# Kernel optimization log

Hardware: AMD Instinct MI355X
Metric: run time of the kernel (lower is better)

## Reference

```python
import jax, jax.numpy as jnp
import numpy as np

B, N, K = 4, 1024, 32
C_S, C_Z, C_H, H, PQ, PV = 384, 128, 16, 12, 4, 8
INF, EPS = 1e5, 1e-8
LN_EPS = 1e-5


def _quat_to_rot(q):
    # q: [..., 4] unit quaternions -> [..., 3, 3]
    w, x, y, z = q[..., 0], q[..., 1], q[..., 2], q[..., 3]
    r = jnp.stack([
        1 - 2 * (y * y + z * z), 2 * (x * y - w * z), 2 * (x * z + w * y),
        2 * (x * y + w * z), 1 - 2 * (x * x + z * z), 2 * (y * z - w * x),
        2 * (x * z - w * y), 2 * (y * z + w * x), 1 - 2 * (x * x + y * y),
    ], axis=-1)
    return r.reshape(q.shape[:-1] + (3, 3))


def _layernorm(x, scale, bias):
    m = jnp.mean(x, axis=-1, keepdims=True)
    v = jnp.mean((x - m) ** 2, axis=-1, keepdims=True)
    return (x - m) * jax.lax.rsqrt(v + LN_EPS) * scale + bias


def setup_inputs():
    key = jax.random.key(0)
    ks = jax.random.split(key, 16)
    s = jax.random.normal(ks[0], (B, N, C_S), jnp.float32)
    z = jax.random.normal(ks[1], (B, N, K, C_Z), jnp.float32)
    edge_index = jax.random.randint(ks[2], (B, N, K), 0, N, jnp.int32)
    quat = jax.random.normal(ks[3], (B, N, 4), jnp.float32)
    rot = _quat_to_rot(quat / jnp.linalg.norm(quat, axis=-1, keepdims=True))
    trans = 10.0 * jax.random.normal(ks[4], (B, N, 3), jnp.float32)
    s_mask = jnp.ones((B, N), jnp.float32)
    sc_s, sc_z = C_S ** -0.5, C_Z ** -0.5
    return {
        "s": s, "z": z, "edge_index": edge_index, "rot": rot, "trans": trans,
        "s_mask": s_mask,
        "ln_s_scale": jnp.ones((C_S,), jnp.float32),
        "ln_s_bias": jnp.zeros((C_S,), jnp.float32),
        "ln_z_scale": jnp.ones((C_Z,), jnp.float32),
        "ln_z_bias": jnp.zeros((C_Z,), jnp.float32),
        "w_q": sc_s * jax.random.normal(ks[5], (C_S, H * C_H), jnp.float32),
        "w_k": sc_s * jax.random.normal(ks[6], (C_S, H * C_H), jnp.float32),
        "w_v": sc_s * jax.random.normal(ks[7], (C_S, H * C_H), jnp.float32),
        "w_q_pts": sc_s * jax.random.normal(ks[8], (C_S, H * PQ * 3), jnp.float32),
        "w_kv_pts": sc_s * jax.random.normal(ks[9], (C_S, H * (PQ + PV) * 3), jnp.float32),
        "w_b": sc_z * jax.random.normal(ks[10], (C_Z, H), jnp.float32),
        "w_down_z": sc_z * jax.random.normal(ks[11], (C_Z, C_Z // 4), jnp.float32),
        "head_weights": jnp.full((H,), 0.541324854612918, jnp.float32),  # softplus^-1(1)
        "w_out": (H * 80) ** -0.5 * jax.random.normal(ks[12], (H * (C_Z // 4 + C_H + PV * 4), C_S), jnp.float32),
    }


def reference(s, z, edge_index, rot, trans, s_mask, ln_s_scale, ln_s_bias,
              ln_z_scale, ln_z_bias, w_q, w_k, w_v, w_q_pts, w_kv_pts, w_b,
              w_down_z, head_weights, w_out):
    bidx = jnp.arange(B)[:, None, None]
    s_ln = _layernorm(s, ln_s_scale, ln_s_bias)          # [B,N,C_S]
    z_ln = _layernorm(z, ln_z_scale, ln_z_bias)          # [B,N,K,C_Z]

    q = (s_ln @ w_q).reshape(B, N, H, C_H)
    k = (s_ln @ w_k)[bidx, edge_index].reshape(B, N, K, H, C_H)
    v = (s_ln @ w_v)[bidx, edge_index].reshape(B, N, K, H, C_H)

    # query points in global frame (query residue's rigid)
    q_pts = (s_ln @ w_q_pts).reshape(B, N, H * PQ, 3)
    q_pts = jnp.einsum('bnij,bnpj->bnpi', rot, q_pts) + trans[:, :, None]
    q_pts = q_pts.reshape(B, N, H, PQ, 3)

    # kv points: gather neighbor local points, then (as in source) apply the
    # QUERY residue's rigid r[..., None, None]
    kv = (s_ln @ w_kv_pts)[bidx, edge_index].reshape(B, N, K, H * (PQ + PV), 3)
    kv = jnp.einsum('bnij,bnkpj->bnkpi', rot, kv) + trans[:, :, None, None]
    kv = kv.reshape(B, N, K, H, PQ + PV, 3)
    k_pts, v_pts = kv[..., :PQ, :], kv[..., PQ:, :]

    b_bias = z_ln @ w_b                                   # [B,N,K,H]
    a = jnp.einsum('bnhc,bnkhc->bnkh', q, k) * (1.0 / (3 * C_H)) ** 0.5
    a = a + (1.0 / 3.0) ** 0.5 * b_bias

    disp = q_pts[:, :, None] - k_pts                      # [B,N,K,H,PQ,3]
    sq = jnp.sum(disp * disp, axis=-1)                    # [B,N,K,H,PQ]
    hw = jax.nn.softplus(head_weights) * (1.0 / (3 * (PQ * 9.0 / 2))) ** 0.5
    a = a - 0.5 * jnp.sum(sq * hw[:, None], axis=-1)      # [B,N,K,H]

    m = s_mask[:, :, None] * s_mask[bidx, edge_index]     # [B,N,K]
    a = a + (INF * (m - 1.0))[..., None]

    a = jax.nn.softmax(jnp.swapaxes(a, -1, -2), axis=-1)  # [B,N,H,K]

    o = jnp.einsum('bnhk,bnkhc->bnhc', a, v).reshape(B, N, H * C_H)

    o_pt = jnp.einsum('bnhk,bnkhvc->bnhvc', a, v_pts)     # [B,N,H,PV,3]
    o_pt = jnp.einsum('bnji,bnhvj->bnhvi', rot, o_pt - trans[:, :, None, None])
    dists = jnp.sqrt(jnp.sum(o_pt * o_pt, axis=-1) + EPS).reshape(B, N, H * PV)
    o_pt_flat = o_pt.reshape(B, N, H * PV * 3)

    o_pair = jnp.einsum('bnhk,bnkc->bnhc', a, z_ln @ w_down_z).reshape(B, N, -1)

    out = jnp.concatenate([o, o_pt_flat, dists, o_pair], axis=-1) @ w_out
    return out
```

## Files before the change

kernel.cpp:

```cpp
#include <hip/hip_runtime.h>
#include <hip/hip_bf16.h>

constexpr int Bb = 4, Nn = 1024, Kk = 32;
constexpr int CS = 384, CZ = 128, CH = 16, Hh = 12, PQn = 4, PVn = 8;
constexpr int HC = Hh * CH;
constexpr int NCOLS = 1152;
constexpr int FEAT = 960;
constexpr int NNODE = Bb * Nn;
constexpr int NEDGE = NNODE * Kk;
constexpr int ZOC = 44;

constexpr int O_WNODE = 4;
constexpr int O_WOUT  = O_WNODE + 384 * 1152;
constexpr int O_WZP   = O_WOUT + 960 * 384;
constexpr int O_BVEC  = O_WZP + 128 * 48;
constexpr int O_CSUM  = O_BVEC + 48;
constexpr int O_SLN   = O_CSUM + 48;
constexpr int O_P     = O_SLN + NNODE * CS;
constexpr int O_ZOUT  = O_P + NNODE * NCOLS;
constexpr int O_FEAT  = O_ZOUT + NEDGE * ZOC;
constexpr int TOTAL_F = O_FEAT + NNODE * FEAT;

__device__ __forceinline__ float ldf(const float* p, int i) { return p[i]; }
__device__ __forceinline__ float ldf(const __hip_bfloat16* p, int i) { return __bfloat162float(p[i]); }
__device__ __forceinline__ void stf(float* p, int i, float v) { p[i] = v; }
__device__ __forceinline__ void stf(__hip_bfloat16* p, int i, float v) { p[i] = __float2bfloat16(v); }
__device__ __forceinline__ float4 ld4(const float* p, int i) { return *(const float4*)(p + i); }
__device__ __forceinline__ float4 ld4(const __hip_bfloat16* p, int i) {
    ushort4 u = *(const ushort4*)(p + i);
    return make_float4(__uint_as_float((unsigned)u.x << 16),
                       __uint_as_float((unsigned)u.y << 16),
                       __uint_as_float((unsigned)u.z << 16),
                       __uint_as_float((unsigned)u.w << 16));
}

__global__ void k_detect(const unsigned* smask_raw, int* flag) {
    if (threadIdx.x == 0) *flag = (smask_raw[0] == 0x3F803F80u) ? 1 : 0;
}

template <typename T>
__global__ __launch_bounds__(384) void k_prep(const T* s, const T* lns_sc, const T* lns_bi,
                                              const T* wq, const T* wk, const T* wv,
                                              const T* wqp, const T* wkvp, const T* wout,
                                              const T* wb, const T* wdz, const T* zsc, const T* zbi,
                                              float* wsf, const int* flag, int want) {
    if (flag && *flag != want) return;
    int blk = blockIdx.x, t = threadIdx.x;
    __shared__ float ssum[6], ssq[6];
    if (blk < 2112) {
        int idx = blk * 384 + t;
        if (idx < 384 * 1152) {
            int row = idx / 1152, col = idx - row * 1152;
            float v;
            if      (col < 192) v = ldf(wq,  row * 192 + col);
            else if (col < 384) v = ldf(wk,  row * 192 + col - 192);
            else if (col < 576) v = ldf(wv,  row * 192 + col - 384);
            else if (col < 720) v = ldf(wqp, row * 144 + col - 576);
            else                v = ldf(wkvp, row * 432 + col - 720);
            wsf[O_WNODE + idx] = v;
        } else {
            int u = idx - 384 * 1152;
            wsf[O_WOUT + u] = ldf(wout, u);
        }
    } else if (blk < 2112 + 4096) {
        int row = blk - 2112;
        float x = ldf(s, row * CS + t);
        float sum = x, sq = x * x;
        #pragma unroll
        for (int m = 32; m; m >>= 1) { sum += __shfl_xor(sum, m, 64); sq += __shfl_xor(sq, m, 64); }
        int w = t >> 6;
        if ((t & 63) == 0) { ssum[w] = sum; ssq[w] = sq; }
        __syncthreads();
        if (t == 0) {
            float S = 0, Q = 0;
            for (int i = 0; i < 6; i++) { S += ssum[i]; Q += ssq[i]; }
            ssum[0] = S; ssq[0] = Q;
        }
        __syncthreads();
        float mean = ssum[0] * (1.f / CS);
        float var  = ssq[0] * (1.f / CS) - mean * mean;
        float r = rsqrtf(var + 1e-5f);
        wsf[O_SLN + row * CS + t] = (x - mean) * r * ldf(lns_sc, t) + ldf(lns_bi, t);
    } else {
        if (t < 128) {
            float sc = ldf(zsc, t);
            for (int o = 0; o < 48; o++) {
                float w = 0.f;
                if (o < 12)      w = ldf(wb, t * 12 + o);
                else if (o < 44) w = ldf(wdz, t * 32 + o - 12);
                wsf[O_WZP + t * 48 + o] = sc * w;
            }
        } else if (t < 176) {
            int o = t - 128;
            float acc = 0.f;
            if (o < 44)
                for (int c = 0; c < 128; c++)
                    acc += ldf(zbi, c) * (o < 12 ? ldf(wb, c * 12 + o) : ldf(wdz, c * 32 + o - 12));
            wsf[O_BVEC + o] = acc;
        } else if (t < 224) {
            int o = t - 176;
            float acc = 0.f;
            if (o < 44)
                for (int c = 0; c < 128; c++)
                    acc += ldf(zsc, c) * (o < 12 ? ldf(wb, c * 12 + o) : ldf(wdz, c * 32 + o - 12));
            wsf[O_CSUM + o] = acc;
        }
    }
}

template <typename T>
__global__ __launch_bounds__(256) void k_zg(const T* z, const float* wzp, const float* bvec,
                                            const float* csum, float* zout,
                                            const int* flag, int want) {
    if (flag && *flag != want) return;
    __shared__ float Ws[128 * 48];
    __shared__ float As[16][260];
    __shared__ float mus[256], rss[256];
    int t = threadIdx.x;
    int edge0 = blockIdx.x * 256;
    for (int i = t; i < 128 * 48; i += 256) Ws[i] = wzp[i];
    int tm = t >> 2, tn = t & 3, col = tn * 12;
    int sr = t >> 2, q = t & 3;
    float psum[4] = {}, psq[4] = {};
    float acc[4][12] = {};
    for (int kt = 0; kt < CZ; kt += 16) {
        float4 zv[4];
        #pragma unroll
        for (int u = 0; u < 4; u++) {
            zv[u] = ld4(z, (edge0 + sr + 64 * u) * CZ + kt + q * 4);
            psum[u] += zv[u].x + zv[u].y + zv[u].z + zv[u].w;
            psq[u]  += zv[u].x * zv[u].x + zv[u].y * zv[u].y
                     + zv[u].z * zv[u].z + zv[u].w * zv[u].w;
        }
        __syncthreads();
        #pragma unroll
        for (int u = 0; u < 4; u++) {
            int rr = sr + 64 * u;
            As[q * 4 + 0][rr] = zv[u].x;
            As[q * 4 + 1][rr] = zv[u].y;
            As[q * 4 + 2][rr] = zv[u].z;
            As[q * 4 + 3][rr] = zv[u].w;
        }
        __syncthreads();
        #pragma unroll
        for (int kk = 0; kk < 16; kk++) {
            float4 a = *(const float4*)&As[kk][tm * 4];
            const float* wr = &Ws[(kt + kk) * 48 + col];
            float4 b0 = *(const float4*)(wr);
            float4 b1 = *(const float4*)(wr + 4);
            float4 b2 = *(const float4*)(wr + 8);
            float av[4]  = {a.x, a.y, a.z, a.w};
            float bv[12] = {b0.x, b0.y, b0.z, b0.w, b1.x, b1.y, b1.z, b1.w, b2.x, b2.y, b2.z, b2.w};
            #pragma unroll
            for (int i = 0; i < 4; i++)
                #pragma unroll
                for (int j = 0; j < 12; j++) acc[i][j] += av[i] * bv[j];
        }
        __syncthreads();
    }
    #pragma unroll
    for (int u = 0; u < 4; u++) {
        float s = psum[u], qq = psq[u];
        s += __shfl_xor(s, 1, 64); s += __shfl_xor(s, 2, 64);
        qq += __shfl_xor(qq, 1, 64); qq += __shfl_xor(qq, 2, 64);
        if (q == 0) {
            float mu = s * (1.f / CZ);
            mus[sr + 64 * u] = mu;
            rss[sr + 64 * u] = rsqrtf(qq * (1.f / CZ) - mu * mu + 1e-5f);
        }
    }
    __syncthreads();
    #pragma unroll
    for (int i = 0; i < 4; i++) {
        int r = tm * 4 + i;
        float mu = mus[r], rs = rss[r];
        int e = edge0 + r;
        #pragma unroll
        for (int j = 0; j < 12; j++) {
            int c = col + j;
            if (c < ZOC) zout[(size_t)e * ZOC + c] = rs * acc[i][j] - rs * mu * csum[c] + bvec[c];
        }
    }
}

__global__ __launch_bounds__(256) void k_gemm(const float* A, int lda, const float* Bm, int ldb,
                                              float* C, int ldc, int Kdim) {
    __shared__ float As[16][68];
    __shared__ float Bs[16][136];
    int t = threadIdx.x;
    int row0 = blockIdx.x * 64, col0 = blockIdx.y * 128;
    int tx = t & 15, ty = t >> 4;
    int ar = t >> 2, aq = t & 3;
    int bk = t >> 4, bc = (t & 15) * 8;
    float acc[4][8] = {};
    for (int kt = 0; kt < Kdim; kt += 16) {
        float4 a0 = *(const float4*)(A + (size_t)(row0 + ar) * lda + kt + aq * 4);
        float4 b0 = *(const float4*)(Bm + (size_t)(kt + bk) * ldb + col0 + bc);
        float4 b1 = *(const float4*)(Bm + (size_t)(kt + bk) * ldb + col0 + bc + 4);
        __syncthreads();
        As[aq * 4 + 0][ar] = a0.x; As[aq * 4 + 1][ar] = a0.y;
        As[aq * 4 + 2][ar] = a0.z; As[aq * 4 + 3][ar] = a0.w;
        *(float4*)&Bs[bk][bc] = b0;
        *(float4*)&Bs[bk][bc + 4] = b1;
        __syncthreads();
        #pragma unroll
        for (int kk = 0; kk < 16; kk++) {
            float4 av  = *(const float4*)&As[kk][ty * 4];
            float4 blo = *(const float4*)&Bs[kk][tx * 4];
            float4 bhi = *(const float4*)&Bs[kk][64 + tx * 4];
            float aa[4] = {av.x, av.y, av.z, av.w};
            float bb[8] = {blo.x, blo.y, blo.z, blo.w, bhi.x, bhi.y, bhi.z, bhi.w};
            #pragma unroll
            for (int i = 0; i < 4; i++)
                #pragma unroll
                for (int j = 0; j < 8; j++)
                    acc[i][j] += aa[i] * bb[j];
        }
    }
    #pragma unroll
    for (int i = 0; i < 4; i++) {
        float* Cr = C + (size_t)(row0 + ty * 4 + i) * ldc + col0;
        *(float4*)(Cr + tx * 4)      = make_float4(acc[i][0], acc[i][1], acc[i][2], acc[i][3]);
        *(float4*)(Cr + 64 + tx * 4) = make_float4(acc[i][4], acc[i][5], acc[i][6], acc[i][7]);
    }
}

template <typename TO>
__global__ __launch_bounds__(256) void k_gout(const float* A, const float* Bm, TO* C,
                                              const int* flag, int want) {
    if (flag && *flag != want) return;
    __shared__ float As[16][36];
    __shared__ float Bs[16][68];
    int t = threadIdx.x;
    int row0 = blockIdx.x * 32, col0 = blockIdx.y * 64;
    int ar = (t >> 2) & 31, aq = t & 3;
    int bk = t >> 4, bc = (t & 15) * 4;
    int ty = t >> 4, tx = t & 15;
    int m0 = ty * 2, n0 = tx * 4;
    float acc[2][4] = {};
    for (int kt = 0; kt < FEAT; kt += 16) {
        float4 av = {};
        if (t < 128) av = *(const float4*)(A + (size_t)(row0 + ar) * FEAT + kt + aq * 4);
        float4 bv = *(const float4*)(Bm + (size_t)(kt + bk) * CS + col0 + bc);
        __syncthreads();
        if (t < 128) {
            As[aq * 4 + 0][ar] = av.x; As[aq * 4 + 1][ar] = av.y;
            As[aq * 4 + 2][ar] = av.z; As[aq * 4 + 3][ar] = av.w;
        }
        *(float4*)&Bs[bk][bc] = bv;
        __syncthreads();
        #pragma unroll
        for (int kk = 0; kk < 16; kk++) {
            float a0 = As[kk][m0], a1 = As[kk][m0 + 1];
            float4 b = *(const float4*)&Bs[kk][n0];
            acc[0][0] += a0 * b.x; acc[0][1] += a0 * b.y; acc[0][2] += a0 * b.z; acc[0][3] += a0 * b.w;
            acc[1][0] += a1 * b.x; acc[1][1] += a1 * b.y; acc[1][2] += a1 * b.z; acc[1][3] += a1 * b.w;
        }
        __syncthreads();
    }
    #pragma unroll
    for (int i = 0; i < 2; i++)
        #pragma unroll
        for (int j = 0; j < 4; j++)
            stf(C, (size_t)(row0 + m0 + i) * CS + col0 + n0 + j, acc[i][j]);
}

template <typename T>
__global__ __launch_bounds__(256) void k_attn(const float* P, const float* zout,
                                              const int* eidx, const T* smask, const T* rot,
                                              const T* hwq, float* featg, const int* flag, int want) {
    if (flag && *flag != want) return;
    __shared__ float nds[4][1760];
    __shared__ int js[4][32];
    int bid = blockIdx.x;
    int nb = ((bid & 7) << 7) + (bid >> 3);
    int w = threadIdx.x >> 6, lane = threadIdx.x & 63;
    int node = nb * 4 + w;
    int b = node >> 10;
    float* S = nds[w];
    int* J = js[w];
    const float* Pn = P + (size_t)node * NCOLS;
    for (int u = lane; u < 336; u += 64)
        S[u] = (u < 192) ? Pn[u] : Pn[384 + u];
    if (lane < 32) {
        int j = eidx[node * Kk + lane];
        J[lane] = b * Nn + j;
        S[360 + lane] = ldf(smask, node) * ldf(smask, b * Nn + j);
    } else if (lane < 44) {
        int h = lane - 32;
        float x = ldf(hwq, h);
        S[336 + h] = logf(1.f + expf(x)) * 0.13608276348795434f;
    } else if (lane < 53) {
        int u = lane - 44;
        int i = u / 3, jj = u - i * 3;
        float m = 0;
        #pragma unroll
        for (int l = 0; l < 3; l++)
            m += ldf(rot, node * 9 + l * 3 + i) * ldf(rot, node * 9 + l * 3 + jj);
        S[348 + u] = m;
    }
    __builtin_amdgcn_wave_barrier();
    #pragma unroll
    for (int it = 0; it < 6; it++) {
        int u = lane + 64 * it;
        int h = u >> 5, k = u & 31;
        const float* Pj = P + (size_t)J[k] * NCOLS;
        float qk = 0;
        const float4* pk4 = (const float4*)(Pj + 192 + h * 16);
        const float4* qs4 = (const float4*)(S + h * 16);
        #pragma unroll
        for (int c4 = 0; c4 < 4; c4++) {
            float4 pv = pk4[c4], qv = qs4[c4];
            qk += qv.x * pv.x + qv.y * pv.y + qv.z * pv.z + qv.w * pv.w;
        }
        float M00 = S[348], M01 = S[349], M02 = S[350],
              M11 = S[352], M12 = S[353], M22 = S[356];
        const float4* pp4 = (const float4*)(Pj + 720 + h * 36);
        const float4* qp4 = (const float4*)(S + 192 + h * 12);
        float4 A0 = pp4[0], A1 = pp4[1], A2 = pp4[2];
        float4 B0 = qp4[0], B1 = qp4[1], B2 = qp4[2];
        float d[12] = {B0.x - A0.x, B0.y - A0.y, B0.z - A0.z, B0.w - A0.w,
                       B1.x - A1.x, B1.y - A1.y, B1.z - A1.z, B1.w - A1.w,
                       B2.x - A2.x, B2.y - A2.y, B2.z - A2.z, B2.w - A2.w};
        float sq = 0;
        #pragma unroll
        for (int p = 0; p < 4; p++) {
            float d0 = d[p * 3], d1 = d[p * 3 + 1], d2 = d[p * 3 + 2];
            sq += M00 * d0 * d0 + M11 * d1 * d1 + M22 * d2 * d2
                + 2.f * (M01 * d0 * d1 + M02 * d0 * d2 + M12 * d1 * d2);
        }
        float logit = qk * 0.14433756729740643f
                    + 0.5773502691896258f * zout[((size_t)node * Kk + k) * ZOC + h]
                    - 0.5f * S[336 + h] * sq
                    + 1e5f * (S[360 + k] - 1.f);
        float mx = logit;
        #pragma unroll
        for (int m = 16; m; m >>= 1) mx = fmaxf(mx, __shfl_xor(mx, m, 64));
        float e = expf(logit - mx);
        float ssum = e;
        #pragma unroll
        for (int m = 16; m; m >>= 1) ssum += __shfl_xor(ssum, m, 64);
        S[392 + h * 33 + k] = e / ssum;
    }
    __builtin_amdgcn_wave_barrier();
    for (int u = lane; u < 216; u += 64) {
        int h, off, fbase, pair = 0;
        if (u < 48)       { h = u >> 2; off = 384 + h * 16 + (u & 3) * 4; fbase = h * 16 + (u & 3) * 4; }
        else if (u < 120) { int v = u - 48;  h = v / 6; int q = v - h * 6;
                            off = 732 + h * 36 + q * 4; fbase = 192 + h * 24 + q * 4; }
        else              { int v = u - 120; h = v >> 3;
                            off = 12 + (v & 7) * 4; fbase = 576 + h * 32 + (v & 7) * 4; pair = 1; }
        float4 acc = {0.f, 0.f, 0.f, 0.f};
        const float* lrow = S + 392 + h * 33;
        if (!pair) {
            #pragma unroll 8
            for (int k = 0; k < 32; k++) {
                float lw = lrow[k];
                float4 pv = *(const float4*)(P + (size_t)J[k] * NCOLS + off);
                acc.x += lw * pv.x; acc.y += lw * pv.y; acc.z += lw * pv.z; acc.w += lw * pv.w;
            }
        } else {
            const float* zr = zout + (size_t)node * Kk * ZOC + off;
            #pragma unroll 8
            for (int k = 0; k < 32; k++) {
                float lw = lrow[k];
                float4 pv = *(const float4*)(zr + k * ZOC);
                acc.x += lw * pv.x; acc.y += lw * pv.y; acc.z += lw * pv.z; acc.w += lw * pv.w;
            }
        }
        *(float4*)&S[788 + fbase] = acc;
    }
    __builtin_amdgcn_wave_barrier();
    for (int u = lane; u < 96; u += 64) {
        float r0 = S[788 + 192 + u * 3 + 0];
        float r1 = S[788 + 192 + u * 3 + 1];
        float r2 = S[788 + 192 + u * 3 + 2];
        float o0 = S[348] * r0 + S[349] * r1 + S[350] * r2;
        float o1 = S[351] * r0 + S[352] * r1 + S[353] * r2;
        float o2 = S[354] * r0 + S[355] * r1 + S[356] * r2;
        S[788 + 192 + u * 3 + 0] = o0;
        S[788 + 192 + u * 3 + 1] = o1;
        S[788 + 192 + u * 3 + 2] = o2;
        S[788 + 480 + u] = sqrtf(o0 * o0 + o1 * o1 + o2 * o2 + 1e-8f);
    }
    __builtin_amdgcn_wave_barrier();
    float* og = featg + (size_t)node * FEAT;
    for (int u = lane; u < 240; u += 64)
        *(float4*)(og + u * 4) = *(const float4*)&S[788 + u * 4];
}

extern "C" void kernel_launch(void* const* d_in, const int* in_sizes, int n_in,
                              void* d_out, int out_size, void* d_ws, size_t ws_size,
                              hipStream_t stream) {
    float* wsf = (float*)d_ws;
    int* flag = (int*)d_ws;
    const void* s = d_in[0];   const void* z = d_in[1];
    const int* eidx = (const int*)d_in[2];
    const void* rot = d_in[3];
    const void* smask = d_in[5];
    const void* lns_sc = d_in[6]; const void* lns_bi = d_in[7];
    const void* lnz_sc = d_in[8]; const void* lnz_bi = d_in[9];
    const void* wq = d_in[10]; const void* wk = d_in[11]; const void* wv = d_in[12];
    const void* wqp = d_in[13]; const void* wkvp = d_in[14];
    const void* wb = d_in[15]; const void* wdz = d_in[16];
    const void* hwq = d_in[17]; const void* wout = d_in[18];

    int mode = -1;
    if (in_sizes) {
        if (in_sizes[0] == NNODE * CS * 4) mode = 0;
        else if (in_sizes[0] == NNODE * CS * 2) mode = 1;
    }

    const int* fg = (mode < 0) ? flag : nullptr;
    if (mode < 0) k_detect<<<1, 64, 0, stream>>>((const unsigned*)smask, flag);

    #define LAUNCH_T(T, WANT)                                                                     \
        do {                                                                                      \
            k_prep<T><<<2112 + 4096 + 1, 384, 0, stream>>>((const T*)s, (const T*)lns_sc,         \
                (const T*)lns_bi, (const T*)wq, (const T*)wk, (const T*)wv, (const T*)wqp,        \
                (const T*)wkvp, (const T*)wout, (const T*)wb, (const T*)wdz, (const T*)lnz_sc,    \
                (const T*)lnz_bi, wsf, fg, WANT);                                                 \
            k_zg<T><<<NEDGE / 256, 256, 0, stream>>>((const T*)z, wsf + O_WZP, wsf + O_BVEC,      \
                wsf + O_CSUM, wsf + O_ZOUT, fg, WANT);                                            \
        } while (0)

    #define LAUNCH_ATTN(T, WANT)                                                                  \
        k_attn<T><<<NNODE / 4, 256, 0, stream>>>(wsf + O_P, wsf + O_ZOUT, eidx,                   \
            (const T*)smask, (const T*)rot, (const T*)hwq, wsf + O_FEAT, fg, WANT)

    if (mode == 0) {
        LAUNCH_T(float, 0);
    } else if (mode == 1) {
        LAUNCH_T(__hip_bfloat16, 1);
    } else {
        LAUNCH_T(float, 0);
        LAUNCH_T(__hip_bfloat16, 1);
    }

    k_gemm<<<dim3(NNODE / 64, NCOLS / 128), 256, 0, stream>>>(
        wsf + O_SLN, CS, wsf + O_WNODE, NCOLS, wsf + O_P, NCOLS, CS);

    if (mode == 0) {
        LAUNCH_ATTN(float, 0);
        k_gout<float><<<dim3(NNODE / 32, CS / 64), 256, 0, stream>>>(
            wsf + O_FEAT, wsf + O_WOUT, (float*)d_out, fg, 0);
    } else if (mode == 1) {
        LAUNCH_ATTN(__hip_bfloat16, 1);
        k_gout<__hip_bfloat16><<<dim3(NNODE / 32, CS / 64), 256, 0, stream>>>(
            wsf + O_FEAT, wsf + O_WOUT, (__hip_bfloat16*)d_out, fg, 1);
    } else {
        LAUNCH_ATTN(float, 0);
        LAUNCH_ATTN(__hip_bfloat16, 1);
        k_gout<float><<<dim3(NNODE / 32, CS / 64), 256, 0, stream>>>(
            wsf + O_FEAT, wsf + O_WOUT, (float*)d_out, fg, 0);
        k_gout<__hip_bfloat16><<<dim3(NNODE / 32, CS / 64), 256, 0, stream>>>(
            wsf + O_FEAT, wsf + O_WOUT, (__hip_bfloat16*)d_out, fg, 1);
    }
    #undef LAUNCH_T
    #undef LAUNCH_ATTN
}
```

Baseline: 376.7 us.

## Replace FP32 SIMT GEMMs with split-bf16 three-pass MFMA GEMMs

The node projection and output projection GEMMs move from FP32 FMA tiling to a 64-thread MFMA kernel. Each operand is split into high and low bf16 halves, and three 32x32x16 bf16 MFMA products are summed to keep near-FP32 accuracy. Weights are pre-transposed into K-contiguous hi/lo buffers, and the LayerNorm output and attention features are emitted as hi/lo pairs. This aims to use matrix cores instead of vector ALUs, at the cost of three MFMAs per tile step and small blocks with no LDS reuse that rely on cache.

```diff
diff --git a/kernel.cpp b/kernel.cpp
--- a/kernel.cpp
+++ b/kernel.cpp
@@ -3,28 +3,34 @@
 
 constexpr int Bb = 4, Nn = 1024, Kk = 32;
 constexpr int CS = 384, CZ = 128, CH = 16, Hh = 12, PQn = 4, PVn = 8;
-constexpr int HC = Hh * CH;
 constexpr int NCOLS = 1152;
 constexpr int FEAT = 960;
 constexpr int NNODE = Bb * Nn;
 constexpr int NEDGE = NNODE * Kk;
 constexpr int ZOC = 44;
 
-constexpr int O_WNODE = 4;
-constexpr int O_WOUT  = O_WNODE + 384 * 1152;
-constexpr int O_WZP   = O_WOUT + 960 * 384;
-constexpr int O_BVEC  = O_WZP + 128 * 48;
+constexpr int O_WZP   = 4;
+constexpr int O_BVEC  = O_WZP + 6144;
 constexpr int O_CSUM  = O_BVEC + 48;
-constexpr int O_SLN   = O_CSUM + 48;
-constexpr int O_P     = O_SLN + NNODE * CS;
+constexpr int O_P     = O_CSUM + 48;
 constexpr int O_ZOUT  = O_P + NNODE * NCOLS;
-constexpr int O_FEAT  = O_ZOUT + NEDGE * ZOC;
-constexpr int TOTAL_F = O_FEAT + NNODE * FEAT;
+constexpr int O_SLNH  = O_ZOUT + NEDGE * ZOC;
+constexpr int O_SLNL  = O_SLNH + NNODE * CS / 2;
+constexpr int O_WNTH  = O_SLNL + NNODE * CS / 2;
+constexpr int O_WNTL  = O_WNTH + NCOLS * CS / 2;
+constexpr int O_WOTH  = O_WNTL + NCOLS * CS / 2;
+constexpr int O_WOTL  = O_WOTH + CS * FEAT / 2;
+constexpr int O_FEATH = O_SLNH;
+constexpr int O_FEATL = O_WOTL + CS * FEAT / 2;
+constexpr int TOTAL_F = O_FEATL + NNODE * FEAT / 2;
+
+typedef __attribute__((ext_vector_type(8)))  short short8x;
+typedef __attribute__((ext_vector_type(16))) float f32x16;
 
 __device__ __forceinline__ float ldf(const float* p, int i) { return p[i]; }
 __device__ __forceinline__ float ldf(const __hip_bfloat16* p, int i) { return __bfloat162float(p[i]); }
-__device__ __forceinline__ void stf(float* p, int i, float v) { p[i] = v; }
-__device__ __forceinline__ void stf(__hip_bfloat16* p, int i, float v) { p[i] = __float2bfloat16(v); }
+__device__ __forceinline__ void stf(float* p, size_t i, float v) { p[i] = v; }
+__device__ __forceinline__ void stf(__hip_bfloat16* p, size_t i, float v) { p[i] = __float2bfloat16(v); }
 __device__ __forceinline__ float4 ld4(const float* p, int i) { return *(const float4*)(p + i); }
 __device__ __forceinline__ float4 ld4(const __hip_bfloat16* p, int i) {
     ushort4 u = *(const ushort4*)(p + i);
@@ -32,6 +38,11 @@
                        __uint_as_float((unsigned)u.y << 16),
                        __uint_as_float((unsigned)u.z << 16),
                        __uint_as_float((unsigned)u.w << 16));
+}
+__device__ __forceinline__ void split_bf(float v, unsigned short& h, unsigned short& l) {
+    h = (unsigned short)(__float_as_uint(v) >> 16);
+    float r = v - __uint_as_float((unsigned)h << 16);
+    l = (unsigned short)(__float_as_uint(r) >> 16);
 }
 
 __global__ void k_detect(const unsigned* smask_raw, int* flag) {
@@ -46,24 +57,32 @@
                                               float* wsf, const int* flag, int want) {
     if (flag && *flag != want) return;
     int blk = blockIdx.x, t = threadIdx.x;
+    unsigned short* wntH = (unsigned short*)(wsf + O_WNTH);
+    unsigned short* wntL = (unsigned short*)(wsf + O_WNTL);
+    unsigned short* wotH = (unsigned short*)(wsf + O_WOTH);
+    unsigned short* wotL = (unsigned short*)(wsf + O_WOTL);
+    unsigned short* slnH = (unsigned short*)(wsf + O_SLNH);
+    unsigned short* slnL = (unsigned short*)(wsf + O_SLNL);
     __shared__ float ssum[6], ssq[6];
-    if (blk < 2112) {
-        int idx = blk * 384 + t;
-        if (idx < 384 * 1152) {
-            int row = idx / 1152, col = idx - row * 1152;
-            float v;
-            if      (col < 192) v = ldf(wq,  row * 192 + col);
-            else if (col < 384) v = ldf(wk,  row * 192 + col - 192);
-            else if (col < 576) v = ldf(wv,  row * 192 + col - 384);
-            else if (col < 720) v = ldf(wqp, row * 144 + col - 576);
-            else                v = ldf(wkvp, row * 432 + col - 720);
-            wsf[O_WNODE + idx] = v;
-        } else {
-            int u = idx - 384 * 1152;
-            wsf[O_WOUT + u] = ldf(wout, u);
-        }
-    } else if (blk < 2112 + 4096) {
-        int row = blk - 2112;
+    if (blk < 1152) {
+        int n = blk, k = t;
+        float v;
+        if      (n < 192) v = ldf(wq,  k * 192 + n);
+        else if (n < 384) v = ldf(wk,  k * 192 + n - 192);
+        else if (n < 576) v = ldf(wv,  k * 192 + n - 384);
+        else if (n < 720) v = ldf(wqp, k * 144 + n - 576);
+        else              v = ldf(wkvp, k * 432 + n - 720);
+        unsigned short h, l; split_bf(v, h, l);
+        wntH[n * 384 + k] = h; wntL[n * 384 + k] = l;
+    } else if (blk < 1536) {
+        int n = blk - 1152;
+        for (int k = t; k < 960; k += 384) {
+            float v = ldf(wout, k * 384 + n);
+            unsigned short h, l; split_bf(v, h, l);
+            wotH[n * 960 + k] = h; wotL[n * 960 + k] = l;
+        }
+    } else if (blk < 1536 + 4096) {
+        int row = blk - 1536;
         float x = ldf(s, row * CS + t);
         float sum = x, sq = x * x;
         #pragma unroll
@@ -80,7 +99,9 @@
         float mean = ssum[0] * (1.f / CS);
         float var  = ssq[0] * (1.f / CS) - mean * mean;
         float r = rsqrtf(var + 1e-5f);
-        wsf[O_SLN + row * CS + t] = (x - mean) * r * ldf(lns_sc, t) + ldf(lns_bi, t);
+        float y = (x - mean) * r * ldf(lns_sc, t) + ldf(lns_bi, t);
+        unsigned short h, l; split_bf(y, h, l);
+        slnH[row * CS + t] = h; slnL[row * CS + t] = l;
     } else {
         if (t < 128) {
             float sc = ldf(zsc, t);
@@ -183,92 +204,58 @@
     }
 }
 
-__global__ __launch_bounds__(256) void k_gemm(const float* A, int lda, const float* Bm, int ldb,
-                                              float* C, int ldc, int Kdim) {
-    __shared__ float As[16][68];
-    __shared__ float Bs[16][136];
-    int t = threadIdx.x;
-    int row0 = blockIdx.x * 64, col0 = blockIdx.y * 128;
-    int tx = t & 15, ty = t >> 4;
-    int ar = t >> 2, aq = t & 3;
-    int bk = t >> 4, bc = (t & 15) * 8;
-    float acc[4][8] = {};
-    for (int kt = 0; kt < Kdim; kt += 16) {
-        float4 a0 = *(const float4*)(A + (size_t)(row0 + ar) * lda + kt + aq * 4);
-        float4 b0 = *(const float4*)(Bm + (size_t)(kt + bk) * ldb + col0 + bc);
-        float4 b1 = *(const float4*)(Bm + (size_t)(kt + bk) * ldb + col0 + bc + 4);
-        __syncthreads();
-        As[aq * 4 + 0][ar] = a0.x; As[aq * 4 + 1][ar] = a0.y;
-        As[aq * 4 + 2][ar] = a0.z; As[aq * 4 + 3][ar] = a0.w;
-        *(float4*)&Bs[bk][bc] = b0;
-        *(float4*)&Bs[bk][bc + 4] = b1;
-        __syncthreads();
-        #pragma unroll
-        for (int kk = 0; kk < 16; kk++) {
-            float4 av  = *(const float4*)&As[kk][ty * 4];
-            float4 blo = *(const float4*)&Bs[kk][tx * 4];
-            float4 bhi = *(const float4*)&Bs[kk][64 + tx * 4];
-            float aa[4] = {av.x, av.y, av.z, av.w};
-            float bb[8] = {blo.x, blo.y, blo.z, blo.w, bhi.x, bhi.y, bhi.z, bhi.w};
-            #pragma unroll
-            for (int i = 0; i < 4; i++)
-                #pragma unroll
-                for (int j = 0; j < 8; j++)
-                    acc[i][j] += aa[i] * bb[j];
-        }
-    }
-    #pragma unroll
-    for (int i = 0; i < 4; i++) {
-        float* Cr = C + (size_t)(row0 + ty * 4 + i) * ldc + col0;
-        *(float4*)(Cr + tx * 4)      = make_float4(acc[i][0], acc[i][1], acc[i][2], acc[i][3]);
-        *(float4*)(Cr + 64 + tx * 4) = make_float4(acc[i][4], acc[i][5], acc[i][6], acc[i][7]);
-    }
-}
+#define MFMA3(C, AH, AL, BH, BL)                                              \
+    C = __builtin_amdgcn_mfma_f32_32x32x16_bf16(AH, BH, C, 0, 0, 0);          \
+    C = __builtin_amdgcn_mfma_f32_32x32x16_bf16(AH, BL, C, 0, 0, 0);          \
+    C = __builtin_amdgcn_mfma_f32_32x32x16_bf16(AL, BH, C, 0, 0, 0);
 
 template <typename TO>
-__global__ __launch_bounds__(256) void k_gout(const float* A, const float* Bm, TO* C,
+__global__ __launch_bounds__(64) void k_mgemm(const unsigned short* AH, const unsigned short* AL,
+                                              int lda, const unsigned short* BH,
+                                              const unsigned short* BL, int ldb,
+                                              TO* C, int ldc, int Kdim,
                                               const int* flag, int want) {
     if (flag && *flag != want) return;
-    __shared__ float As[16][36];
-    __shared__ float Bs[16][68];
-    int t = threadIdx.x;
-    int row0 = blockIdx.x * 32, col0 = blockIdx.y * 64;
-    int ar = (t >> 2) & 31, aq = t & 3;
-    int bk = t >> 4, bc = (t & 15) * 4;
-    int ty = t >> 4, tx = t & 15;
-    int m0 = ty * 2, n0 = tx * 4;
-    float acc[2][4] = {};
-    for (int kt = 0; kt < FEAT; kt += 16) {
-        float4 av = {};
-        if (t < 128) av = *(const float4*)(A + (size_t)(row0 + ar) * FEAT + kt + aq * 4);
-        float4 bv = *(const float4*)(Bm + (size_t)(kt + bk) * CS + col0 + bc);
-        __syncthreads();
-        if (t < 128) {
-            As[aq * 4 + 0][ar] = av.x; As[aq * 4 + 1][ar] = av.y;
-            As[aq * 4 + 2][ar] = av.z; As[aq * 4 + 3][ar] = av.w;
-        }
-        *(float4*)&Bs[bk][bc] = bv;
-        __syncthreads();
-        #pragma unroll
-        for (int kk = 0; kk < 16; kk++) {
-            float a0 = As[kk][m0], a1 = As[kk][m0 + 1];
-            float4 b = *(const float4*)&Bs[kk][n0];
-            acc[0][0] += a0 * b.x; acc[0][1] += a0 * b.y; acc[0][2] += a0 * b.z; acc[0][3] += a0 * b.w;
-            acc[1][0] += a1 * b.x; acc[1][1] += a1 * b.y; acc[1][2] += a1 * b.z; acc[1][3] += a1 * b.w;
-        }
-        __syncthreads();
+    int l = threadIdx.x, r = l & 31, g = l >> 5;
+    size_t a0 = (size_t)(blockIdx.x * 64 + r) * lda + 8 * g;
+    size_t a1 = a0 + (size_t)32 * lda;
+    size_t b0 = (size_t)(blockIdx.y * 64 + r) * ldb + 8 * g;
+    size_t b1 = b0 + (size_t)32 * ldb;
+    f32x16 c00 = {}, c01 = {}, c10 = {}, c11 = {};
+    short8x aH0 = *(const short8x*)(AH + a0), aH1 = *(const short8x*)(AH + a1);
+    short8x aL0 = *(const short8x*)(AL + a0), aL1 = *(const short8x*)(AL + a1);
+    short8x bH0 = *(const short8x*)(BH + b0), bH1 = *(const short8x*)(BH + b1);
+    short8x bL0 = *(const short8x*)(BL + b0), bL1 = *(const short8x*)(BL + b1);
+    for (int kt = 0; kt < Kdim; kt += 16) {
+        int kn = (kt + 16 < Kdim) ? kt + 16 : 0;
+        short8x nAH0 = *(const short8x*)(AH + a0 + kn), nAH1 = *(const short8x*)(AH + a1 + kn);
+        short8x nAL0 = *(const short8x*)(AL + a0 + kn), nAL1 = *(const short8x*)(AL + a1 + kn);
+        short8x nBH0 = *(const short8x*)(BH + b0 + kn), nBH1 = *(const short8x*)(BH + b1 + kn);
+        short8x nBL0 = *(const short8x*)(BL + b0 + kn), nBL1 = *(const short8x*)(BL + b1 + kn);
+        MFMA3(c00, aH0, aL0, bH0, bL0)
+        MFMA3(c01, aH0, aL0, bH1, bL1)
+        MFMA3(c10, aH1, aL1, bH0, bL0)
+        MFMA3(c11, aH1, aL1, bH1, bL1)
+        aH0 = nAH0; aH1 = nAH1; aL0 = nAL0; aL1 = nAL1;
+        bH0 = nBH0; bH1 = nBH1; bL0 = nBL0; bL1 = nBL1;
     }
     #pragma unroll
-    for (int i = 0; i < 2; i++)
-        #pragma unroll
-        for (int j = 0; j < 4; j++)
-            stf(C, (size_t)(row0 + m0 + i) * CS + col0 + n0 + j, acc[i][j]);
+    for (int reg = 0; reg < 16; reg++) {
+        int row = (reg & 3) + 8 * (reg >> 2) + 4 * g;
+        size_t rm = (size_t)(blockIdx.x * 64 + row);
+        int cn = blockIdx.y * 64 + r;
+        stf(C, rm * ldc + cn,               c00[reg]);
+        stf(C, rm * ldc + cn + 32,          c01[reg]);
+        stf(C, (rm + 32) * ldc + cn,        c10[reg]);
+        stf(C, (rm + 32) * ldc + cn + 32,   c11[reg]);
+    }
 }
 
 template <typename T>
 __global__ __launch_bounds__(256) void k_attn(const float* P, const float* zout,
                                               const int* eidx, const T* smask, const T* rot,
-                                              const T* hwq, float* featg, const int* flag, int want) {
+                                              const T* hwq, unsigned short* featH,
+                                              unsigned short* featL, const int* flag, int want) {
     if (flag && *flag != want) return;
     __shared__ float nds[4][1760];
     __shared__ int js[4][32];
@@ -384,9 +371,11 @@
         S[788 + 480 + u] = sqrtf(o0 * o0 + o1 * o1 + o2 * o2 + 1e-8f);
     }
     __builtin_amdgcn_wave_barrier();
-    float* og = featg + (size_t)node * FEAT;
-    for (int u = lane; u < 240; u += 64)
-        *(float4*)(og + u * 4) = *(const float4*)&S[788 + u * 4];
+    for (int u = lane; u < FEAT; u += 64) {
+        unsigned short h, l; split_bf(S[788 + u], h, l);
+        featH[(size_t)node * FEAT + u] = h;
+        featL[(size_t)node * FEAT + u] = l;
+    }
 }
 
 extern "C" void kernel_launch(void* const* d_in, const int* in_sizes, int n_in,
@@ -405,57 +394,60 @@
     const void* wb = d_in[15]; const void* wdz = d_in[16];
     const void* hwq = d_in[17]; const void* wout = d_in[18];
 
+    unsigned short* slnH = (unsigned short*)(wsf + O_SLNH);
+    unsigned short* slnL = (unsigned short*)(wsf + O_SLNL);
+    unsigned short* wntH = (unsigned short*)(wsf + O_WNTH);
+    unsigned short* wntL = (unsigned short*)(wsf + O_WNTL);
+    unsigned short* wotH = (unsigned short*)(wsf + O_WOTH);
+    unsigned short* wotL = (unsigned short*)(wsf + O_WOTL);
+    unsigned short* featH = (unsigned short*)(wsf + O_FEATH);
+    unsigned short* featL = (unsigned short*)(wsf + O_FEATL);
+
     int mode = -1;
     if (in_sizes) {
         if (in_sizes[0] == NNODE * CS * 4) mode = 0;
         else if (in_sizes[0] == NNODE * CS * 2) mode = 1;
     }
-
     const int* fg = (mode < 0) ? flag : nullptr;
     if (mode < 0) k_detect<<<1, 64, 0, stream>>>((const unsigned*)smask, flag);
 
-    #define LAUNCH_T(T, WANT)                                                                     \
+    #define LAUNCH_FRONT(T, WANT)                                                                 \
         do {                                                                                      \
-            k_prep<T><<<2112 + 4096 + 1, 384, 0, stream>>>((const T*)s, (const T*)lns_sc,         \
-                (const T*)lns_bi, (const T*)wq, (const T*)wk, (const T*)wv, (const T*)wqp,        \
-                (const T*)wkvp, (const T*)wout, (const T*)wb, (const T*)wdz, (const T*)lnz_sc,    \
-                (const T*)lnz_bi, wsf, fg, WANT);                                                 \
+            k_prep<T><<<5633, 384, 0, stream>>>((const T*)s, (const T*)lns_sc, (const T*)lns_bi,  \
+                (const T*)wq, (const T*)wk, (const T*)wv, (const T*)wqp, (const T*)wkvp,          \
+                (const T*)wout, (const T*)wb, (const T*)wdz, (const T*)lnz_sc, (const T*)lnz_bi,  \
+                wsf, fg, WANT);                                                                   \
             k_zg<T><<<NEDGE / 256, 256, 0, stream>>>((const T*)z, wsf + O_WZP, wsf + O_BVEC,      \
                 wsf + O_CSUM, wsf + O_ZOUT, fg, WANT);                                            \
         } while (0)
 
     #define LAUNCH_ATTN(T, WANT)                                                                  \
         k_attn<T><<<NNODE / 4, 256, 0, stream>>>(wsf + O_P, wsf + O_ZOUT, eidx,                   \
-            (const T*)smask, (const T*)rot, (const T*)hwq, wsf + O_FEAT, fg, WANT)
-
-    if (mode == 0) {
-        LAUNCH_T(float, 0);
-    } else if (mode == 1) {
-        LAUNCH_T(__hip_bfloat16, 1);
-    } else {
-        LAUNCH_T(float, 0);
-        LAUNCH_T(__hip_bfloat16, 1);
-    }
-
-    k_gemm<<<dim3(NNODE / 64, NCOLS / 128), 256, 0, stream>>>(
-        wsf + O_SLN, CS, wsf + O_WNODE, NCOLS, wsf + O_P, NCOLS, CS);
+            (const T*)smask, (const T*)rot, (const T*)hwq, featH, featL, fg, WANT)
+
+    if (mode == 0)      LAUNCH_FRONT(float, 0);
+    else if (mode == 1) LAUNCH_FRONT(__hip_bfloat16, 1);
+    else { LAUNCH_FRONT(float, 0); LAUNCH_FRONT(__hip_bfloat16, 1); }
+
+    k_mgemm<float><<<dim3(NNODE / 64, NCOLS / 64), 64, 0, stream>>>(
+        slnH, slnL, CS, wntH, wntL, CS, wsf + O_P, NCOLS, CS, nullptr, 0);
 
     if (mode == 0) {
         LAUNCH_ATTN(float, 0);
-        k_gout<float><<<dim3(NNODE / 32, CS / 64), 256, 0, stream>>>(
-            wsf + O_FEAT, wsf + O_WOUT, (float*)d_out, fg, 0);
+        k_mgemm<float><<<dim3(NNODE / 64, CS / 64), 64, 0, stream>>>(
+            featH, featL, FEAT, wotH, wotL, FEAT, (float*)d_out, CS, FEAT, nullptr, 0);
     } else if (mode == 1) {
         LAUNCH_ATTN(__hip_bfloat16, 1);
-        k_gout<__hip_bfloat16><<<dim3(NNODE / 32, CS / 64), 256, 0, stream>>>(
-            wsf + O_FEAT, wsf + O_WOUT, (__hip_bfloat16*)d_out, fg, 1);
+        k_mgemm<__hip_bfloat16><<<dim3(NNODE / 64, CS / 64), 64, 0, stream>>>(
+            featH, featL, FEAT, wotH, wotL, FEAT, (__hip_bfloat16*)d_out, CS, FEAT, nullptr, 0);
     } else {
         LAUNCH_ATTN(float, 0);
         LAUNCH_ATTN(__hip_bfloat16, 1);
-        k_gout<float><<<dim3(NNODE / 32, CS / 64), 256, 0, stream>>>(
-            wsf + O_FEAT, wsf + O_WOUT, (float*)d_out, fg, 0);
-        k_gout<__hip_bfloat16><<<dim3(NNODE / 32, CS / 64), 256, 0, stream>>>(
-            wsf + O_FEAT, wsf + O_WOUT, (__hip_bfloat16*)d_out, fg, 1);
-    }
-    #undef LAUNCH_T
+        k_mgemm<float><<<dim3(NNODE / 64, CS / 64), 64, 0, stream>>>(
+            featH, featL, FEAT, wotH, wotL, FEAT, (float*)d_out, CS, FEAT, fg, 0);
+        k_mgemm<__hip_bfloat16><<<dim3(NNODE / 64, CS / 64), 64, 0, stream>>>(
+            featH, featL, FEAT, wotH, wotL, FEAT, (__hip_bfloat16*)d_out, CS, FEAT, fg, 1);
+    }
+    #undef LAUNCH_FRONT
     #undef LAUNCH_ATTN
 }
```

Result: faster. 345.9 us (-8.2%).
